# Kernel tuning notes

Hardware: AMD Instinct MI355X
Metric: run time of the kernel (lower is better)

Reference implementation:

```python
import jax, jax.numpy as jnp
import numpy as np

H = 2048          # hidden_size
I = 1024          # moe_intermediate_size
E = 32            # n_routed_experts
K = 4             # num_experts_per_tok
N_SHARED = 1
EPS = 1e-6


def setup_inputs() -> dict:
    key = jax.random.key(0)
    ks = jax.random.split(key, 8)
    s = 1.0 / np.sqrt(H)
    si = 1.0 / np.sqrt(I)
    return {
        "hidden_states": jax.random.normal(ks[0], (1, 4096, H), jnp.float32),
        "norm_w": jnp.ones((H,), jnp.float32),
        "gate_w": jax.random.normal(ks[1], (E, H), jnp.float32) * s,      # MoEGate.weight
        "w13": jax.random.normal(ks[2], (E, H, 2 * I), jnp.float32) * s,  # fused w1w3
        "w2": jax.random.normal(ks[3], (E, I, H), jnp.float32) * si,      # fused w2
        "shared_gate_w": jax.random.normal(ks[4], (H, I * N_SHARED), jnp.float32) * s,
        "shared_up_w": jax.random.normal(ks[5], (H, I * N_SHARED), jnp.float32) * s,
        "shared_down_w": jax.random.normal(ks[6], (I * N_SHARED, H), jnp.float32) * si,
    }


def _rmsnorm(x, w, eps=EPS):
    var = jnp.mean(jnp.square(x), axis=-1, keepdims=True)
    return x * jax.lax.rsqrt(var + eps) * w


def _moe_core(x, gate_w, w13, w2):
    # x: [T, H] (post-norm tokens)
    T = x.shape[0]
    N = T * K
    C = 2 * N // E

    # --- gate (fp32, F.linear) ---
    logits = jnp.einsum("th,eh->te", x.astype(jnp.float32), gate_w.astype(jnp.float32))
    scores = jax.nn.softmax(logits, axis=-1)
    topk_w, topk_ids = jax.lax.top_k(scores, K)           # [T, K]
    topk_w = topk_w / jnp.sum(topk_w, axis=-1, keepdims=True)  # norm_topk_prob

    # --- dispatch: sort token-expert pairs by expert ---
    flat_ids = topk_ids.reshape(-1)                        # [N] int
    flat_w = topk_w.reshape(-1)                            # [N]
    order = jnp.argsort(flat_ids)                          # stable sort by expert
    sorted_eid = flat_ids[order]                           # [N]
    tok = order // K                                       # source token per sorted slot
    counts = jnp.zeros((E,), jnp.int32).at[flat_ids].add(1)  # tokens_per_expert
    starts = jnp.cumsum(counts) - counts
    pos = jnp.arange(N) - starts[sorted_eid]               # position within expert group

    # scatter tokens into [E, C, H] buffer (OOB rows dropped; C sized so this ~never happens)
    buf = jnp.zeros((E, C, x.shape[1]), x.dtype).at[sorted_eid, pos].set(x[tok], mode="drop")

    # --- grouped expert FFN (swiglu) ---
    gu = jnp.einsum("ech,ehf->ecf", buf, w13)              # [E, C, 2I]
    g, u = jnp.split(gu, 2, axis=-1)
    act = jax.nn.silu(g) * u                               # swiglu
    eo = jnp.einsum("eci,eih->ech", act, w2)               # [E, C, H]

    # --- combine: gather back and weighted scatter-add per source token ---
    out_slots = eo[sorted_eid, pos]                        # [N, H]
    routed = jnp.zeros_like(x).at[tok].add(out_slots * flat_w[order][:, None])
    return routed


def reference(hidden_states, norm_w, gate_w, w13, w2, shared_gate_w, shared_up_w, shared_down_w):
    B, S, Hd = hidden_states.shape
    residual = hidden_states
    h = _rmsnorm(hidden_states, norm_w)                    # post_attention_layernorm
    x = h.reshape(-1, Hd)                                  # [T, H]

    routed = _moe_core(x, gate_w, w13, w2)                 # routed experts output

    # shared experts MLP (swiglu)
    shared = (jax.nn.silu(x @ shared_gate_w) * (x @ shared_up_w)) @ shared_down_w

    out = residual + (routed + shared).reshape(B, S, Hd)
    return out
```

## Files before the change

kernel.cpp:

```cpp
#include <hip/hip_runtime.h>
#include <hip/hip_bf16.h>
#include <math.h>

#define HD 2048
#define ID 1024
#define NE 32
#define TOPK 4
#define NTOK 4096
#define NSLOT (NTOK*TOPK)

typedef __attribute__((ext_vector_type(4))) float f32x4;
typedef __attribute__((ext_vector_type(8))) short bf16x8;
typedef unsigned short u16;
typedef unsigned int u32;

union U32x4BF { uint4 u; bf16x8 h; };

static __device__ __forceinline__ u16 f2bf(float f) {
  union { float f; u32 u; } v; v.f = f;
  u32 r = v.u + 0x7fffu + ((v.u >> 16) & 1u);
  return (u16)(r >> 16);
}

static __device__ __forceinline__ u32 cvtpk(float lo, float hi) {
  u32 r;
  asm("v_cvt_pk_bf16_f32 %0, %1, %2" : "=v"(r) : "v"(lo), "v"(hi));
  return r;
}

static __device__ __forceinline__ void barrier_lgkm() {
  asm volatile("s_waitcnt lgkmcnt(0)" ::: "memory");
  __builtin_amdgcn_s_barrier();
}

__global__ __launch_bounds__(256) void k_rmsnorm(const float* __restrict__ x,
                                                 const float* __restrict__ w,
                                                 u16* __restrict__ xn,
                                                 float* __restrict__ out) {
  int t = blockIdx.x, tid = threadIdx.x;
  const float* row = x + (size_t)t * HD;
  float4 v0 = ((const float4*)row)[tid*2+0];
  float4 v1 = ((const float4*)row)[tid*2+1];
  float* orow = out + (size_t)t * HD;
  ((float4*)orow)[tid*2+0] = v0;
  ((float4*)orow)[tid*2+1] = v1;
  float ss = v0.x*v0.x+v0.y*v0.y+v0.z*v0.z+v0.w*v0.w
           + v1.x*v1.x+v1.y*v1.y+v1.z*v1.z+v1.w*v1.w;
  #pragma unroll
  for (int d=1; d<64; d<<=1) ss += __shfl_xor(ss, d);
  __shared__ float red[4];
  if ((tid&63)==0) red[tid>>6] = ss;
  __syncthreads();
  float rs = rsqrtf((red[0]+red[1]+red[2]+red[3]) * (1.0f/HD) + 1e-6f);
  const float* wp = w + tid*8;
  float a[8] = {v0.x,v0.y,v0.z,v0.w,v1.x,v1.y,v1.z,v1.w};
  uint4 o;
  o.x = (u32)f2bf(a[0]*rs*wp[0]) | ((u32)f2bf(a[1]*rs*wp[1])<<16);
  o.y = (u32)f2bf(a[2]*rs*wp[2]) | ((u32)f2bf(a[3]*rs*wp[3])<<16);
  o.z = (u32)f2bf(a[4]*rs*wp[4]) | ((u32)f2bf(a[5]*rs*wp[5])<<16);
  o.w = (u32)f2bf(a[6]*rs*wp[6]) | ((u32)f2bf(a[7]*rs*wp[7])<<16);
  ((uint4*)xn)[(size_t)t*(HD/8) + tid] = o;
}

__global__ __launch_bounds__(256) void k_gate(const float* __restrict__ x,
                                              const float* __restrict__ w,
                                              const float* __restrict__ gw,
                                              int* __restrict__ topk_id,
                                              float* __restrict__ topk_w,
                                              int* __restrict__ counts) {
  __shared__ float xs[HD];
  __shared__ float red[4];
  __shared__ float logits[NE];
  int t = blockIdx.x, tid = threadIdx.x;
  const float* row = x + (size_t)t*HD;
  float4 v0 = ((const float4*)row)[tid*2+0];
  float4 v1 = ((const float4*)row)[tid*2+1];
  float ss = v0.x*v0.x+v0.y*v0.y+v0.z*v0.z+v0.w*v0.w
           + v1.x*v1.x+v1.y*v1.y+v1.z*v1.z+v1.w*v1.w;
  #pragma unroll
  for (int d=1; d<64; d<<=1) ss += __shfl_xor(ss, d);
  if ((tid&63)==0) red[tid>>6] = ss;
  __syncthreads();
  float rs = 1.0f / sqrtf((red[0]+red[1]+red[2]+red[3]) * (1.0f/HD) + 1e-6f);
  const float* wp = w + tid*8;
  float a[8] = {v0.x,v0.y,v0.z,v0.w,v1.x,v1.y,v1.z,v1.w};
  #pragma unroll
  for (int j=0;j<8;++j) xs[tid*8+j] = a[j]*rs*wp[j];
  __syncthreads();
  int wave = tid>>6, lane = tid&63;
  for (int ei=0; ei<8; ++ei) {
    int e = wave*8 + ei;
    const float* g = gw + (size_t)e*HD;
    float s = 0.f;
    #pragma unroll
    for (int j=0;j<HD/64;++j) s += xs[lane + j*64] * g[lane + j*64];
    #pragma unroll
    for (int d=1; d<64; d<<=1) s += __shfl_xor(s, d);
    if (lane==0) logits[e] = s;
  }
  __syncthreads();
  if (tid==0) {
    float best[TOPK]; int bid[TOPK]; unsigned used = 0;
    for (int k2=0;k2<TOPK;++k2) {
      float bv = -1e30f; int bi = 0;
      for (int i2=0;i2<NE;++i2)
        if (!((used>>i2)&1u) && logits[i2] > bv) { bv = logits[i2]; bi = i2; }
      used |= 1u<<bi; best[k2] = bv; bid[k2] = bi;
    }
    float mx = best[0], sum = 0.f, wv[TOPK];
    for (int k2=0;k2<TOPK;++k2) { wv[k2] = expf(best[k2]-mx); sum += wv[k2]; }
    float inv = 1.f/sum;
    for (int k2=0;k2<TOPK;++k2) {
      topk_id[t*TOPK+k2] = bid[k2];
      topk_w[t*TOPK+k2] = wv[k2]*inv;
      atomicAdd(&counts[bid[k2]], 1);
    }
  }
}

__global__ void k_zero(int* counts, int* cursors) {
  int i = threadIdx.x;
  if (i < NE) { counts[i] = 0; cursors[i] = 0; }
}

__global__ void k_scan(const int* __restrict__ counts, int* __restrict__ starts) {
  if (threadIdx.x==0 && blockIdx.x==0) {
    int acc = 0;
    for (int e=0;e<NE;++e) { starts[e] = acc; acc += counts[e]; }
  }
}

__global__ __launch_bounds__(256) void k_dispatch(const int* __restrict__ topk_id,
                                                  const float* __restrict__ topk_w,
                                                  const int* __restrict__ starts,
                                                  int* __restrict__ cursors,
                                                  int* __restrict__ slot_tok,
                                                  float* __restrict__ slot_w) {
  int i = blockIdx.x*256 + threadIdx.x;
  int e = topk_id[i];
  int p = atomicAdd(&cursors[e], 1);
  int slot = starts[e] + p;
  slot_tok[slot] = i >> 2;
  slot_w[slot] = topk_w[i];
}

static __device__ __forceinline__ void packB(u16* Bb, int tq, int kb, const float4* bv) {
  int h = tq & 15;
  #pragma unroll
  for (int j = 0; j < 4; ++j) {
    int p = 2*tq + (j>>1);
    int cpar = j & 1;
    int s0 = ((4*kb + 0 + cpar) ^ h) * 4;
    int s1 = ((4*kb + 2 + cpar) ^ h) * 4;
    uint2 w0, w1;
    w0.x = cvtpk(((const float*)&bv[0])[j], ((const float*)&bv[1])[j]);
    w0.y = cvtpk(((const float*)&bv[2])[j], ((const float*)&bv[3])[j]);
    w1.x = cvtpk(((const float*)&bv[4])[j], ((const float*)&bv[5])[j]);
    w1.y = cvtpk(((const float*)&bv[6])[j], ((const float*)&bv[7])[j]);
    *(uint2*)&Bb[p*64 + s0] = w0;
    *(uint2*)&Bb[p*64 + s1] = w1;
  }
}

static __device__ __forceinline__ void loadB8(const float* bsrc, int ldb, float4* bv) {
  #pragma unroll
  for (int i = 0; i < 8; ++i) bv[i] = *(const float4*)(bsrc + (size_t)i*ldb);
}

__global__ __launch_bounds__(256, 2) void k_gemm_up(
    const u16* __restrict__ A, const float* __restrict__ w13,
    const float* __restrict__ sgw, const float* __restrict__ suw,
    const int* __restrict__ counts, const int* __restrict__ starts,
    const int* __restrict__ slot_tok,
    u16* __restrict__ act, u16* __restrict__ sact) {
  __shared__ u16 Al[2][4096];
  __shared__ u16 Bl[2][8192];
  __shared__ int rowL[128];
  int t = threadIdx.x;
  int n0 = blockIdx.x * 128;
  int m0 = blockIdx.y * 128;
  int e  = blockIdx.z;
  bool routed = (e < NE);
  int M, rowbase;
  u16* actOut;
  if (routed) { M = counts[e]; rowbase = starts[e]; actOut = act; if (m0 >= M) return; }
  else { M = NTOK; rowbase = 0; actOut = sact; }
  if (t < 128) {
    int m = m0 + t;
    rowL[t] = routed ? slot_tok[rowbase + (m < M ? m : M-1)] : m;
  }
  __syncthreads();
  int r0i = t>>2;
  int segA = ((t&3) ^ ((r0i>>1)&3)) << 3;
  const u16* srcA0 = A + (size_t)rowL[r0i]*HD + segA;
  const u16* srcA1 = A + (size_t)rowL[r0i+64]*HD + segA;
  int tq = t & 63, kb = t >> 6;
  int sc4 = tq * 4;
  int isup = (sc4 >> 4) & 1;
  int og = ((sc4 >> 5) << 4) | (sc4 & 15);
  int ldb;
  const float* bsrc;
  if (routed) {
    ldb = 2*ID;
    const float* base = w13 + (size_t)e*HD*2*ID + (isup ? ID : 0);
    bsrc = base + (size_t)(kb*8)*ldb + (n0 + og);
  } else {
    ldb = ID;
    const float* base = isup ? suw : sgw;
    bsrc = base + (size_t)(kb*8)*ldb + (n0 + og);
  }

  int lane = t&63, wn = t>>6;
  int l15 = lane&15, l4 = lane>>4;
  int aoffb = l15*32 + ((l4 ^ ((l15>>1)&3))<<3);
  int b0off[4];
  #pragma unroll
  for (int fn=0; fn<4; ++fn) {
    int pbase = wn*32 + fn*8 + (l15>>1);
    int h = (fn*4 + (l15>>2)) & 15;
    b0off[fn] = pbase*64 + (((4*l4 + (l15&1)) ^ h) << 2);
  }
  f32x4 acc[8][4];
  #pragma unroll
  for (int fm=0;fm<8;++fm)
    #pragma unroll
    for (int fn=0;fn<4;++fn)
      acc[fm][fn] = (f32x4){0.f,0.f,0.f,0.f};

  uint4 aA0 = *(const uint4*)srcA0, aA1 = *(const uint4*)srcA1;
  float4 bv[8]; loadB8(bsrc, ldb, bv);
  srcA0 += 32; srcA1 += 32; bsrc += (size_t)32*ldb;
  *(uint4*)&Al[0][t*8] = aA0;
  *(uint4*)&Al[0][2048 + t*8] = aA1;
  packB(Bl[0], tq, kb, bv);
  barrier_lgkm();

  int cur = 0;
  const int kiter = HD/32;
  for (int kt = 0; kt < kiter; ++kt) {
    bool more = (kt+1 < kiter);
    if (more) {
      aA0 = *(const uint4*)srcA0; aA1 = *(const uint4*)srcA1;
      loadB8(bsrc, ldb, bv);
      srcA0 += 32; srcA1 += 32; bsrc += (size_t)32*ldb;
    }
    {
      bf16x8 bfr[4];
      #pragma unroll
      for (int fn=0; fn<4; ++fn) {
        uint2 lo = *(const uint2*)&Bl[cur][b0off[fn]];
        uint2 hi = *(const uint2*)&Bl[cur][b0off[fn] ^ 8];
        U32x4BF ub; ub.u = make_uint4(lo.x, lo.y, hi.x, hi.y);
        bfr[fn] = ub.h;
      }
      __builtin_amdgcn_s_setprio(1);
      #pragma unroll
      for (int fm=0; fm<8; ++fm) {
        bf16x8 af = *(const bf16x8*)&Al[cur][aoffb + fm*512];
        #pragma unroll
        for (int fn=0; fn<4; ++fn)
          acc[fm][fn] = __builtin_amdgcn_mfma_f32_16x16x32_bf16(af, bfr[fn], acc[fm][fn], 0,0,0);
      }
      __builtin_amdgcn_s_setprio(0);
    }
    if (more) {
      *(uint4*)&Al[cur^1][t*8] = aA0;
      *(uint4*)&Al[cur^1][2048 + t*8] = aA1;
      packB(Bl[cur^1], tq, kb, bv);
    }
    cur ^= 1;
    barrier_lgkm();
  }
  #pragma unroll
  for (int fm=0; fm<8; ++fm) {
    #pragma unroll
    for (int fq=0; fq<2; ++fq) {
      f32x4 g = acc[fm][2*fq], u = acc[fm][2*fq+1];
      int col = n0 + (wn*2+fq)*16 + l15;
      #pragma unroll
      for (int r=0;r<4;++r) {
        int mloc = fm*16 + l4*4 + r;
        int m = m0 + mloc;
        if (m < M) {
          float gv = g[r];
          float av = gv / (1.f + expf(-gv)) * u[r];
          actOut[(size_t)(rowbase+m)*ID + col] = f2bf(av);
        }
      }
    }
  }
}

__global__ __launch_bounds__(256, 2) void k_gemm_down(
    const u16* __restrict__ act, const u16* __restrict__ sact,
    const float* __restrict__ w2, const float* __restrict__ sdw,
    const int* __restrict__ counts, const int* __restrict__ starts,
    const int* __restrict__ slot_tok, const float* __restrict__ slot_w,
    float* __restrict__ out) {
  __shared__ u16 Al[2][4096];
  __shared__ u16 Bl[2][8192];
  __shared__ int tokL[128];
  __shared__ float wL[128];
  int t = threadIdx.x;
  int n0 = blockIdx.x * 256;
  int m0 = blockIdx.y * 128;
  int e  = blockIdx.z;
  bool routed = (e < NE);
  int M, rowbase;
  const u16* A;
  if (routed) { M = counts[e]; rowbase = starts[e]; A = act; if (m0 >= M) return; }
  else { M = NTOK; rowbase = 0; A = sact; }
  if (routed && t < 128) {
    int m = m0 + t;
    tokL[t] = (m<M) ? slot_tok[rowbase+m] : 0;
    wL[t]   = (m<M) ? slot_w[rowbase+m]  : 0.f;
  }
  if (routed) __syncthreads();
  int r0i = t>>2;
  int segA = ((t&3) ^ ((r0i>>1)&3)) << 3;
  int am0 = m0 + r0i, am1 = m0 + r0i + 64;
  const u16* srcA0 = A + (size_t)(rowbase + (am0 < M ? am0 : M-1))*ID + segA;
  const u16* srcA1 = A + (size_t)(rowbase + (am1 < M ? am1 : M-1))*ID + segA;
  int tq = t & 63, kb = t >> 6;
  int sc4 = tq * 4;
  const float* bsrc = (routed ? (w2 + (size_t)e*ID*HD) : sdw)
                    + (size_t)(kb*8)*HD + (n0 + sc4);

  int lane = t&63, wn = t>>6;
  int l15 = lane&15, l4 = lane>>4;
  int aoffb = l15*32 + ((l4 ^ ((l15>>1)&3))<<3);
  int b0off[4];
  #pragma unroll
  for (int fn=0; fn<4; ++fn) {
    int pbase = wn*32 + fn*8 + (l15>>1);
    int h = (fn*4 + (l15>>2)) & 15;
    b0off[fn] = pbase*64 + (((4*l4 + (l15&1)) ^ h) << 2);
  }
  f32x4 acc[8][4];
  #pragma unroll
  for (int fm=0;fm<8;++fm)
    #pragma unroll
    for (int fn=0;fn<4;++fn)
      acc[fm][fn] = (f32x4){0.f,0.f,0.f,0.f};

  uint4 aA0 = *(const uint4*)srcA0, aA1 = *(const uint4*)srcA1;
  float4 bv[8]; loadB8(bsrc, HD, bv);
  srcA0 += 32; srcA1 += 32; bsrc += (size_t)32*HD;
  *(uint4*)&Al[0][t*8] = aA0;
  *(uint4*)&Al[0][2048 + t*8] = aA1;
  packB(Bl[0], tq, kb, bv);
  barrier_lgkm();

  int cur = 0;
  const int kiter = ID/32;
  for (int kt = 0; kt < kiter; ++kt) {
    bool more = (kt+1 < kiter);
    if (more) {
      aA0 = *(const uint4*)srcA0; aA1 = *(const uint4*)srcA1;
      loadB8(bsrc, HD, bv);
      srcA0 += 32; srcA1 += 32; bsrc += (size_t)32*HD;
    }
    {
      bf16x8 bfr[4];
      #pragma unroll
      for (int fn=0; fn<4; ++fn) {
        uint2 lo = *(const uint2*)&Bl[cur][b0off[fn]];
        uint2 hi = *(const uint2*)&Bl[cur][b0off[fn] ^ 8];
        U32x4BF ub; ub.u = make_uint4(lo.x, lo.y, hi.x, hi.y);
        bfr[fn] = ub.h;
      }
      __builtin_amdgcn_s_setprio(1);
      #pragma unroll
      for (int fm=0; fm<8; ++fm) {
        bf16x8 af = *(const bf16x8*)&Al[cur][aoffb + fm*512];
        #pragma unroll
        for (int fn=0; fn<4; ++fn)
          acc[fm][fn] = __builtin_amdgcn_mfma_f32_16x16x32_bf16(af, bfr[fn], acc[fm][fn], 0,0,0);
      }
      __builtin_amdgcn_s_setprio(0);
    }
    if (more) {
      *(uint4*)&Al[cur^1][t*8] = aA0;
      *(uint4*)&Al[cur^1][2048 + t*8] = aA1;
      packB(Bl[cur^1], tq, kb, bv);
    }
    cur ^= 1;
    barrier_lgkm();
  }
  #pragma unroll
  for (int fm=0; fm<8; ++fm) {
    #pragma unroll
    for (int fn=0; fn<4; ++fn) {
      f32x4 v = acc[fm][fn];
      int col = n0 + wn*64 + fn*16 + l15;
      #pragma unroll
      for (int r=0;r<4;++r) {
        int mloc = fm*16 + l4*4 + r;
        int m = m0 + mloc;
        if (m < M) {
          if (routed) {
            atomicAdd(&out[(size_t)tokL[mloc]*HD + col], v[r]*wL[mloc]);
          } else {
            atomicAdd(&out[(size_t)m*HD + col], v[r]);
          }
        }
      }
    }
  }
}

extern "C" void kernel_launch(void* const* d_in, const int* in_sizes, int n_in,
                              void* d_out, int out_size, void* d_ws, size_t ws_size,
                              hipStream_t stream) {
  const float* x    = (const float*)d_in[0];
  const float* nw   = (const float*)d_in[1];
  const float* gw   = (const float*)d_in[2];
  const float* w13  = (const float*)d_in[3];
  const float* w2   = (const float*)d_in[4];
  const float* sgw  = (const float*)d_in[5];
  const float* suw  = (const float*)d_in[6];
  const float* sdw  = (const float*)d_in[7];
  float* out = (float*)d_out;

  char* p = (char*)d_ws;
  u16* xn   = (u16*)p;  p += (size_t)NTOK*HD*2;
  u16* act  = (u16*)p;  p += (size_t)NSLOT*ID*2;
  u16* sact = (u16*)p;  p += (size_t)NTOK*ID*2;
  int*   topk_id  = (int*)p;   p += (size_t)NTOK*TOPK*4;
  float* topk_w   = (float*)p; p += (size_t)NTOK*TOPK*4;
  int*   slot_tok = (int*)p;   p += (size_t)NSLOT*4;
  float* slot_w   = (float*)p; p += (size_t)NSLOT*4;
  int*   counts   = (int*)p;   p += 64*4;
  int*   cursors  = (int*)p;   p += 64*4;
  int*   starts   = (int*)p;   p += 64*4;

  k_zero<<<1, 64, 0, stream>>>(counts, cursors);
  k_rmsnorm<<<NTOK, 256, 0, stream>>>(x, nw, xn, out);
  k_gate<<<NTOK, 256, 0, stream>>>(x, nw, gw, topk_id, topk_w, counts);
  k_scan<<<1, 1, 0, stream>>>(counts, starts);
  k_dispatch<<<NSLOT/256, 256, 0, stream>>>(topk_id, topk_w, starts, cursors, slot_tok, slot_w);

  k_gemm_up<<<dim3(ID/128, 32, NE+1), 256, 0, stream>>>(
      xn, w13, sgw, suw, counts, starts, slot_tok, act, sact);
  k_gemm_down<<<dim3(HD/256, 32, NE+1), 256, 0, stream>>>(
      act, sact, w2, sdw, counts, starts, slot_tok, slot_w, out);
}
```

Baseline: 758.8 us.

## Load fp32 weight B fragments directly into registers, bypassing LDS staging

The up and down grouped GEMMs no longer stage converted bf16 weight tiles in shared memory. Each lane now loads the scalar fp32 weights it needs for its MFMA B-fragments straight from global memory and converts them to bf16 in registers. The A pipeline is reworked into a two-stage register prefetch over an unrolled pair of k-steps. This removes the LDS B writes and reads and frees LDS, but swaps coalesced float4 loads for strided scalar loads (8 rows per lane) and raises register pressure at 2 blocks per CU.

```diff
diff --git a/kernel.cpp b/kernel.cpp
--- a/kernel.cpp
+++ b/kernel.cpp
@@ -31,6 +31,31 @@
 static __device__ __forceinline__ void barrier_lgkm() {
   asm volatile("s_waitcnt lgkmcnt(0)" ::: "memory");
   __builtin_amdgcn_s_barrier();
+}
+
+static __device__ __forceinline__ void loadBreg(const float* __restrict__ bg,
+                                                const float* __restrict__ bu,
+                                                u32 o0, u32 o1, u32 o2, u32 o3,
+                                                u32 ldb, float bs[4][8]) {
+  #pragma unroll
+  for (int j = 0; j < 8; ++j) {
+    bs[0][j] = bg[o0 + j*ldb];
+    bs[1][j] = bu[o1 + j*ldb];
+    bs[2][j] = bg[o2 + j*ldb];
+    bs[3][j] = bu[o3 + j*ldb];
+  }
+}
+
+static __device__ __forceinline__ void cvtB(const float bs[4][8], bf16x8 bfr[4]) {
+  #pragma unroll
+  for (int fn = 0; fn < 4; ++fn) {
+    U32x4BF ub;
+    ub.u.x = cvtpk(bs[fn][0], bs[fn][1]);
+    ub.u.y = cvtpk(bs[fn][2], bs[fn][3]);
+    ub.u.z = cvtpk(bs[fn][4], bs[fn][5]);
+    ub.u.w = cvtpk(bs[fn][6], bs[fn][7]);
+    bfr[fn] = ub.h;
+  }
 }
 
 __global__ __launch_bounds__(256) void k_rmsnorm(const float* __restrict__ x,
@@ -144,29 +169,6 @@
   slot_w[slot] = topk_w[i];
 }
 
-static __device__ __forceinline__ void packB(u16* Bb, int tq, int kb, const float4* bv) {
-  int h = tq & 15;
-  #pragma unroll
-  for (int j = 0; j < 4; ++j) {
-    int p = 2*tq + (j>>1);
-    int cpar = j & 1;
-    int s0 = ((4*kb + 0 + cpar) ^ h) * 4;
-    int s1 = ((4*kb + 2 + cpar) ^ h) * 4;
-    uint2 w0, w1;
-    w0.x = cvtpk(((const float*)&bv[0])[j], ((const float*)&bv[1])[j]);
-    w0.y = cvtpk(((const float*)&bv[2])[j], ((const float*)&bv[3])[j]);
-    w1.x = cvtpk(((const float*)&bv[4])[j], ((const float*)&bv[5])[j]);
-    w1.y = cvtpk(((const float*)&bv[6])[j], ((const float*)&bv[7])[j]);
-    *(uint2*)&Bb[p*64 + s0] = w0;
-    *(uint2*)&Bb[p*64 + s1] = w1;
-  }
-}
-
-static __device__ __forceinline__ void loadB8(const float* bsrc, int ldb, float4* bv) {
-  #pragma unroll
-  for (int i = 0; i < 8; ++i) bv[i] = *(const float4*)(bsrc + (size_t)i*ldb);
-}
-
 __global__ __launch_bounds__(256, 2) void k_gemm_up(
     const u16* __restrict__ A, const float* __restrict__ w13,
     const float* __restrict__ sgw, const float* __restrict__ suw,
@@ -174,7 +176,6 @@
     const int* __restrict__ slot_tok,
     u16* __restrict__ act, u16* __restrict__ sact) {
   __shared__ u16 Al[2][4096];
-  __shared__ u16 Bl[2][8192];
   __shared__ int rowL[128];
   int t = threadIdx.x;
   int n0 = blockIdx.x * 128;
@@ -194,32 +195,30 @@
   int segA = ((t&3) ^ ((r0i>>1)&3)) << 3;
   const u16* srcA0 = A + (size_t)rowL[r0i]*HD + segA;
   const u16* srcA1 = A + (size_t)rowL[r0i+64]*HD + segA;
-  int tq = t & 63, kb = t >> 6;
-  int sc4 = tq * 4;
-  int isup = (sc4 >> 4) & 1;
-  int og = ((sc4 >> 5) << 4) | (sc4 & 15);
-  int ldb;
-  const float* bsrc;
-  if (routed) {
-    ldb = 2*ID;
-    const float* base = w13 + (size_t)e*HD*2*ID + (isup ? ID : 0);
-    bsrc = base + (size_t)(kb*8)*ldb + (n0 + og);
-  } else {
-    ldb = ID;
-    const float* base = isup ? suw : sgw;
-    bsrc = base + (size_t)(kb*8)*ldb + (n0 + og);
-  }
 
   int lane = t&63, wn = t>>6;
   int l15 = lane&15, l4 = lane>>4;
   int aoffb = l15*32 + ((l4 ^ ((l15>>1)&3))<<3);
-  int b0off[4];
-  #pragma unroll
-  for (int fn=0; fn<4; ++fn) {
-    int pbase = wn*32 + fn*8 + (l15>>1);
-    int h = (fn*4 + (l15>>2)) & 15;
-    b0off[fn] = pbase*64 + (((4*l4 + (l15&1)) ^ h) << 2);
-  }
+
+  const float *bbg, *bbu;
+  u32 ldb, o0, o1, o2, o3;
+  {
+    int c0 = n0 + (wn*2+0)*16 + l15;
+    int c1 = n0 + (wn*2+1)*16 + l15;
+    if (routed) {
+      ldb = 2*ID;
+      bbg = w13 + (size_t)e*HD*2*ID; bbu = bbg;
+      u32 rb = (u32)(l4*8)*ldb;
+      o0 = rb + c0; o1 = rb + c0 + ID; o2 = rb + c1; o3 = rb + c1 + ID;
+    } else {
+      ldb = ID;
+      bbg = sgw; bbu = suw;
+      u32 rb = (u32)(l4*8)*ldb;
+      o0 = rb + c0; o1 = rb + c0; o2 = rb + c1; o3 = rb + c1;
+    }
+  }
+  u32 kadv = 32*ldb;
+
   f32x4 acc[8][4];
   #pragma unroll
   for (int fm=0;fm<8;++fm)
@@ -228,48 +227,59 @@
       acc[fm][fn] = (f32x4){0.f,0.f,0.f,0.f};
 
   uint4 aA0 = *(const uint4*)srcA0, aA1 = *(const uint4*)srcA1;
-  float4 bv[8]; loadB8(bsrc, ldb, bv);
-  srcA0 += 32; srcA1 += 32; bsrc += (size_t)32*ldb;
+  srcA0 += 32; srcA1 += 32;
+  float bsA[4][8]; loadBreg(bbg, bbu, o0,o1,o2,o3, ldb, bsA);
+  o0 += kadv; o1 += kadv; o2 += kadv; o3 += kadv;
+  uint4 aB0 = *(const uint4*)srcA0, aB1 = *(const uint4*)srcA1;
+  srcA0 += 32; srcA1 += 32;
+  float bsB[4][8]; loadBreg(bbg, bbu, o0,o1,o2,o3, ldb, bsB);
+  o0 += kadv; o1 += kadv; o2 += kadv; o3 += kadv;
   *(uint4*)&Al[0][t*8] = aA0;
   *(uint4*)&Al[0][2048 + t*8] = aA1;
-  packB(Bl[0], tq, kb, bv);
   barrier_lgkm();
 
-  int cur = 0;
   const int kiter = HD/32;
-  for (int kt = 0; kt < kiter; ++kt) {
-    bool more = (kt+1 < kiter);
-    if (more) {
-      aA0 = *(const uint4*)srcA0; aA1 = *(const uint4*)srcA1;
-      loadB8(bsrc, ldb, bv);
-      srcA0 += 32; srcA1 += 32; bsrc += (size_t)32*ldb;
-    }
+  for (int kt = 0; kt < kiter; kt += 2) {
     {
-      bf16x8 bfr[4];
-      #pragma unroll
-      for (int fn=0; fn<4; ++fn) {
-        uint2 lo = *(const uint2*)&Bl[cur][b0off[fn]];
-        uint2 hi = *(const uint2*)&Bl[cur][b0off[fn] ^ 8];
-        U32x4BF ub; ub.u = make_uint4(lo.x, lo.y, hi.x, hi.y);
-        bfr[fn] = ub.h;
-      }
+      bool pf = (kt+2 < kiter);
+      if (pf) { aA0 = *(const uint4*)srcA0; aA1 = *(const uint4*)srcA1; srcA0 += 32; srcA1 += 32; }
+      bf16x8 bfr[4]; cvtB(bsA, bfr);
+      if (pf) { loadBreg(bbg, bbu, o0,o1,o2,o3, ldb, bsA);
+                o0 += kadv; o1 += kadv; o2 += kadv; o3 += kadv; }
       __builtin_amdgcn_s_setprio(1);
       #pragma unroll
       for (int fm=0; fm<8; ++fm) {
-        bf16x8 af = *(const bf16x8*)&Al[cur][aoffb + fm*512];
+        bf16x8 af = *(const bf16x8*)&Al[0][aoffb + fm*512];
         #pragma unroll
         for (int fn=0; fn<4; ++fn)
           acc[fm][fn] = __builtin_amdgcn_mfma_f32_16x16x32_bf16(af, bfr[fn], acc[fm][fn], 0,0,0);
       }
       __builtin_amdgcn_s_setprio(0);
-    }
-    if (more) {
-      *(uint4*)&Al[cur^1][t*8] = aA0;
-      *(uint4*)&Al[cur^1][2048 + t*8] = aA1;
-      packB(Bl[cur^1], tq, kb, bv);
-    }
-    cur ^= 1;
-    barrier_lgkm();
+      *(uint4*)&Al[1][t*8] = aB0;
+      *(uint4*)&Al[1][2048 + t*8] = aB1;
+      barrier_lgkm();
+    }
+    {
+      bool pf = (kt+3 < kiter);
+      if (pf) { aB0 = *(const uint4*)srcA0; aB1 = *(const uint4*)srcA1; srcA0 += 32; srcA1 += 32; }
+      bf16x8 bfr[4]; cvtB(bsB, bfr);
+      if (pf) { loadBreg(bbg, bbu, o0,o1,o2,o3, ldb, bsB);
+                o0 += kadv; o1 += kadv; o2 += kadv; o3 += kadv; }
+      __builtin_amdgcn_s_setprio(1);
+      #pragma unroll
+      for (int fm=0; fm<8; ++fm) {
+        bf16x8 af = *(const bf16x8*)&Al[1][aoffb + fm*512];
+        #pragma unroll
+        for (int fn=0; fn<4; ++fn)
+          acc[fm][fn] = __builtin_amdgcn_mfma_f32_16x16x32_bf16(af, bfr[fn], acc[fm][fn], 0,0,0);
+      }
+      __builtin_amdgcn_s_setprio(0);
+      if (kt+2 < kiter) {
+        *(uint4*)&Al[0][t*8] = aA0;
+        *(uint4*)&Al[0][2048 + t*8] = aA1;
+      }
+      barrier_lgkm();
+    }
   }
   #pragma unroll
   for (int fm=0; fm<8; ++fm) {
@@ -298,7 +308,6 @@
     const int* __restrict__ slot_tok, const float* __restrict__ slot_w,
     float* __restrict__ out) {
   __shared__ u16 Al[2][4096];
-  __shared__ u16 Bl[2][8192];
   __shared__ int tokL[128];
   __shared__ float wL[128];
   int t = threadIdx.x;
@@ -321,21 +330,20 @@
   int am0 = m0 + r0i, am1 = m0 + r0i + 64;
   const u16* srcA0 = A + (size_t)(rowbase + (am0 < M ? am0 : M-1))*ID + segA;
   const u16* srcA1 = A + (size_t)(rowbase + (am1 < M ? am1 : M-1))*ID + segA;
-  int tq = t & 63, kb = t >> 6;
-  int sc4 = tq * 4;
-  const float* bsrc = (routed ? (w2 + (size_t)e*ID*HD) : sdw)
-                    + (size_t)(kb*8)*HD + (n0 + sc4);
 
   int lane = t&63, wn = t>>6;
   int l15 = lane&15, l4 = lane>>4;
   int aoffb = l15*32 + ((l4 ^ ((l15>>1)&3))<<3);
-  int b0off[4];
-  #pragma unroll
-  for (int fn=0; fn<4; ++fn) {
-    int pbase = wn*32 + fn*8 + (l15>>1);
-    int h = (fn*4 + (l15>>2)) & 15;
-    b0off[fn] = pbase*64 + (((4*l4 + (l15&1)) ^ h) << 2);
-  }
+
+  const float* bb = routed ? (w2 + (size_t)e*ID*HD) : sdw;
+  const u32 ldb = HD;
+  u32 rb = (u32)(l4*8)*ldb;
+  u32 o0 = rb + n0 + wn*64 + 0*16 + l15;
+  u32 o1 = rb + n0 + wn*64 + 1*16 + l15;
+  u32 o2 = rb + n0 + wn*64 + 2*16 + l15;
+  u32 o3 = rb + n0 + wn*64 + 3*16 + l15;
+  const u32 kadv = 32*ldb;
+
   f32x4 acc[8][4];
   #pragma unroll
   for (int fm=0;fm<8;++fm)
@@ -344,48 +352,59 @@
       acc[fm][fn] = (f32x4){0.f,0.f,0.f,0.f};
 
   uint4 aA0 = *(const uint4*)srcA0, aA1 = *(const uint4*)srcA1;
-  float4 bv[8]; loadB8(bsrc, HD, bv);
-  srcA0 += 32; srcA1 += 32; bsrc += (size_t)32*HD;
+  srcA0 += 32; srcA1 += 32;
+  float bsA[4][8]; loadBreg(bb, bb, o0,o1,o2,o3, ldb, bsA);
+  o0 += kadv; o1 += kadv; o2 += kadv; o3 += kadv;
+  uint4 aB0 = *(const uint4*)srcA0, aB1 = *(const uint4*)srcA1;
+  srcA0 += 32; srcA1 += 32;
+  float bsB[4][8]; loadBreg(bb, bb, o0,o1,o2,o3, ldb, bsB);
+  o0 += kadv; o1 += kadv; o2 += kadv; o3 += kadv;
   *(uint4*)&Al[0][t*8] = aA0;
   *(uint4*)&Al[0][2048 + t*8] = aA1;
-  packB(Bl[0], tq, kb, bv);
   barrier_lgkm();
 
-  int cur = 0;
   const int kiter = ID/32;
-  for (int kt = 0; kt < kiter; ++kt) {
-    bool more = (kt+1 < kiter);
-    if (more) {
-      aA0 = *(const uint4*)srcA0; aA1 = *(const uint4*)srcA1;
-      loadB8(bsrc, HD, bv);
-      srcA0 += 32; srcA1 += 32; bsrc += (size_t)32*HD;
-    }
+  for (int kt = 0; kt < kiter; kt += 2) {
     {
-      bf16x8 bfr[4];
-      #pragma unroll
-      for (int fn=0; fn<4; ++fn) {
-        uint2 lo = *(const uint2*)&Bl[cur][b0off[fn]];
-        uint2 hi = *(const uint2*)&Bl[cur][b0off[fn] ^ 8];
-        U32x4BF ub; ub.u = make_uint4(lo.x, lo.y, hi.x, hi.y);
-        bfr[fn] = ub.h;
-      }
+      bool pf = (kt+2 < kiter);
+      if (pf) { aA0 = *(const uint4*)srcA0; aA1 = *(const uint4*)srcA1; srcA0 += 32; srcA1 += 32; }
+      bf16x8 bfr[4]; cvtB(bsA, bfr);
+      if (pf) { loadBreg(bb, bb, o0,o1,o2,o3, ldb, bsA);
+                o0 += kadv; o1 += kadv; o2 += kadv; o3 += kadv; }
       __builtin_amdgcn_s_setprio(1);
       #pragma unroll
       for (int fm=0; fm<8; ++fm) {
-        bf16x8 af = *(const bf16x8*)&Al[cur][aoffb + fm*512];
+        bf16x8 af = *(const bf16x8*)&Al[0][aoffb + fm*512];
         #pragma unroll
         for (int fn=0; fn<4; ++fn)
           acc[fm][fn] = __builtin_amdgcn_mfma_f32_16x16x32_bf16(af, bfr[fn], acc[fm][fn], 0,0,0);
       }
       __builtin_amdgcn_s_setprio(0);
-    }
-    if (more) {
-      *(uint4*)&Al[cur^1][t*8] = aA0;
-      *(uint4*)&Al[cur^1][2048 + t*8] = aA1;
-      packB(Bl[cur^1], tq, kb, bv);
-    }
-    cur ^= 1;
-    barrier_lgkm();
+      *(uint4*)&Al[1][t*8] = aB0;
+      *(uint4*)&Al[1][2048 + t*8] = aB1;
+      barrier_lgkm();
+    }
+    {
+      bool pf = (kt+3 < kiter);
+      if (pf) { aB0 = *(const uint4*)srcA0; aB1 = *(const uint4*)srcA1; srcA0 += 32; srcA1 += 32; }
+      bf16x8 bfr[4]; cvtB(bsB, bfr);
+      if (pf) { loadBreg(bb, bb, o0,o1,o2,o3, ldb, bsB);
+                o0 += kadv; o1 += kadv; o2 += kadv; o3 += kadv; }
+      __builtin_amdgcn_s_setprio(1);
+      #pragma unroll
+      for (int fm=0; fm<8; ++fm) {
+        bf16x8 af = *(const bf16x8*)&Al[1][aoffb + fm*512];
+        #pragma unroll
+        for (int fn=0; fn<4; ++fn)
+          acc[fm][fn] = __builtin_amdgcn_mfma_f32_16x16x32_bf16(af, bfr[fn], acc[fm][fn], 0,0,0);
+      }
+      __builtin_amdgcn_s_setprio(0);
+      if (kt+2 < kiter) {
+        *(uint4*)&Al[0][t*8] = aA0;
+        *(uint4*)&Al[0][2048 + t*8] = aA1;
+      }
+      barrier_lgkm();
+    }
   }
   #pragma unroll
   for (int fm=0; fm<8; ++fm) {
```

New measurement: 752.9 us. About the same (-0.8%).
